# Kernel optimization log

Measured on AMD Instinct MI355X. Metric: run time of the kernel, lower is better.

The kernel has to match this reference:

```python
import jax, jax.numpy as jnp
import numpy as np

NE, NR = 100000, 50
E, H, M = 512, 8, 8
HD = E // H
B = 65536


def setup_inputs() -> dict:
    key = jax.random.key(0)
    ks = jax.random.split(key, 24)
    xav = lambda k, shp: jax.random.normal(k, shp, jnp.float32) * (2.0 / (shp[0] + shp[-1])) ** 0.5
    return {
        'entity_emb': xav(ks[0], (NE, E)),
        'relation_emb': xav(ks[1], (NR, E)),
        'dens_ent_emb': jax.random.normal(ks[2], (NE, E), jnp.float32) * 0.02,
        'dens_ent_w': xav(ks[3], (E, 1)), 'dens_ent_b': jnp.zeros((1,), jnp.float32),
        'dens_rel_emb': jax.random.normal(ks[4], (NR, E), jnp.float32) * 0.02,
        'dens_rel_w': xav(ks[5], (E, 1)), 'dens_rel_b': jnp.zeros((1,), jnp.float32),
        'local_motifs': xav(ks[6], (M, HD)),
        'global_motifs': xav(ks[7], (M, HD)),
        'Wq': xav(ks[8], (E, E)), 'bq': jnp.zeros((E,), jnp.float32),
        'Wkl': xav(ks[9], (HD, HD)), 'bkl': jnp.zeros((HD,), jnp.float32),
        'Wkg': xav(ks[10], (HD, HD)), 'bkg': jnp.zeros((HD,), jnp.float32),
        'Wout': xav(ks[11], (2 * E, E)), 'bout': jnp.zeros((E,), jnp.float32),
        'adv_w': jnp.float32(1.0), 'adv_b': jnp.float32(0.0),
        'h_idx': jax.random.randint(ks[12], (B,), 0, NE),
        'r_idx': jax.random.randint(ks[13], (B,), 0, NR),
        't_idx': jax.random.randint(ks[14], (B,), 0, NE),
    }


def reference(entity_emb, relation_emb, dens_ent_emb, dens_ent_w, dens_ent_b,
              dens_rel_emb, dens_rel_w, dens_rel_b, local_motifs, global_motifs,
              Wq, bq, Wkl, bkl, Wkg, bkg, Wout, bout, adv_w, adv_b,
              h_idx, r_idx, t_idx):
    h = entity_emb[h_idx]           # [B, E]
    r = relation_emb[r_idx]
    t = entity_emb[t_idx]
    # density gating: sigmoid(Linear(Embedding(idx))) per head/tail/relation, averaged
    h_d = jax.nn.sigmoid(dens_ent_emb[h_idx] @ dens_ent_w + dens_ent_b)   # [B,1]
    t_d = jax.nn.sigmoid(dens_ent_emb[t_idx] @ dens_ent_w + dens_ent_b)
    r_d = jax.nn.sigmoid(dens_rel_emb[r_idx] @ dens_rel_w + dens_rel_b)
    density = (h_d + t_d + r_d) / 3.0                                     # [B,1]
    diff = h + r - t
    # hierarchical soft attention over local/global motif codebooks
    ctx = h + r + t
    q = (ctx @ Wq + bq).reshape(-1, H, HD)                                # [B,H,HD]
    lk = local_motifs @ Wkl + bkl                                         # [M,HD]
    gk = global_motifs @ Wkg + bkg
    scale = 1.0 / jnp.sqrt(jnp.asarray(HD, q.dtype))
    dens = density[:, :, None]                                            # [B,1,1]
    l_w = jax.nn.softmax(jnp.einsum('bhd,md->bhm', q, lk) * scale + dens, axis=-1)
    g_w = jax.nn.softmax(jnp.einsum('bhd,md->bhm', q, gk) * scale + dens, axis=-1)
    attn = (l_w + g_w) / 2.0                                              # [B,H,M]
    motifs = local_motifs + global_motifs                                 # [M,HD]
    motif_repr = jnp.einsum('bhm,md->bhd', attn, motifs).reshape(-1, E)   # [B,E]
    motif_loss = jnp.sum((diff - motif_repr) ** 2, axis=-1)               # ||.||^2
    combined = jnp.concatenate([diff, motif_repr], axis=-1)               # [B,2E]
    transformed = jnp.tanh(combined @ Wout + bout)
    score = adv_w * jnp.linalg.norm(transformed, axis=-1) + adv_b
    return score, motif_loss
```

## Files before the change

kernel.cpp:

```cpp
#include <hip/hip_runtime.h>
#include <math.h>

#define B_TOT 65536

typedef __attribute__((ext_vector_type(4))) float f32x4;
typedef __attribute__((ext_vector_type(4))) unsigned int u32x4;
typedef __attribute__((ext_vector_type(8))) __bf16 bf16x8;

#define OFF_WLOGT 0u
#define OFF_CBIAS 131072u
#define OFF_BCAT  131584u
#define OFF_MOTIF 721408u
#define OFF_LK    723456u
#define OFF_GK    725504u
#define OFF_DIFF  1048576u
#define OFF_ATTN  68157440u
#define OFF_SSQ   76546048u

__device__ __forceinline__ unsigned short f2bf(float x) {
  union { float f; unsigned int u; } v; v.f = x;
  return (unsigned short)((v.u + 0x7FFFu + ((v.u >> 16) & 1u)) >> 16);
}

__device__ __forceinline__ float bf2f(unsigned short u) {
  union { unsigned int i; float f; } v; v.i = ((unsigned int)u) << 16; return v.f;
}

__device__ __forceinline__ float fast_tanh(float x) {
  float cx = fminf(fmaxf(x, -15.f), 15.f);
  float e = __expf(2.f * cx);
  return 1.f - 2.f * __builtin_amdgcn_rcpf(e + 1.f);
}

__global__ __launch_bounds__(256) void k0a(
    const float* __restrict__ lm, const float* __restrict__ gm,
    const float* __restrict__ Wkl, const float* __restrict__ bkl,
    const float* __restrict__ Wkg, const float* __restrict__ bkg,
    const float* __restrict__ bq,
    float* __restrict__ lk, float* __restrict__ gk,
    float* __restrict__ motifs, float* __restrict__ cb) {
  int tid = threadIdx.x;
  for (int o = tid; o < 512; o += 256) {
    int m = o >> 6, d = o & 63;
    float s1 = bkl[d], s2 = bkg[d];
    for (int k = 0; k < 64; ++k) {
      s1 += lm[m*64+k] * Wkl[k*64+d];
      s2 += gm[m*64+k] * Wkg[k*64+d];
    }
    lk[o] = s1; gk[o] = s2;
    motifs[o] = lm[o] + gm[o];
  }
  __syncthreads();
  if (tid < 128) {
    int s_ = tid >> 6, h = (tid >> 3) & 7, m = tid & 7;
    const float* K = s_ ? gk : lk;
    float s = 0.f;
    for (int d = 0; d < 64; ++d) s += bq[h*64+d] * K[m*64+d];
    cb[tid] = 0.125f * s;
  }
}

__global__ __launch_bounds__(256) void k0b(
    const float* __restrict__ Wq, const float* __restrict__ Wout,
    const float* __restrict__ lk, const float* __restrict__ gk,
    const float* __restrict__ motifs,
    unsigned short* __restrict__ wlogT, unsigned short* __restrict__ bcatT) {
  int idx = blockIdx.x * 256 + threadIdx.x;
  if (idx >= 65536 + 512*576) return;
  if (idx < 65536) {
    int c = idx >> 9, k = idx & 511;
    int s_ = c >> 6, h = (c >> 3) & 7, m = c & 7;
    const float* K = (s_ ? gk : lk) + m*64;
    const float* wq = Wq + (size_t)k*512 + h*64;
    float s = 0.f;
    for (int d = 0; d < 64; ++d) s += wq[d] * K[d];
    wlogT[(size_t)c*512 + k] = f2bf(0.125f * s);
  } else {
    int i2 = idx - 65536;
    int n = i2 / 576, k = i2 - n*576;
    float v;
    if (k < 512) {
      v = Wout[(size_t)k*512 + n];
    } else {
      int hm = k - 512, h = hm >> 3, m = hm & 7;
      const float* mo = motifs + m*64;
      const float* wo = Wout + (size_t)(512 + h*64)*512 + n;
      v = 0.f;
      for (int d = 0; d < 64; ++d) v += mo[d] * wo[(size_t)d*512];
    }
    bcatT[(size_t)n*576 + k] = f2bf(v);
  }
}

__global__ __launch_bounds__(256, 4) void kA(
    const float* __restrict__ ent, const float* __restrict__ rel,
    const int* __restrict__ hI, const int* __restrict__ rI, const int* __restrict__ tI,
    const unsigned short* __restrict__ wlogT, const float* __restrict__ cb,
    unsigned short* __restrict__ diffB, unsigned short* __restrict__ attnB) {
  __shared__ __align__(16) unsigned char smem[32768];
  unsigned short* As = (unsigned short*)smem;
  unsigned short* Bs = (unsigned short*)(smem + 9216);
  float* lg  = (float*)smem;

  int tid = threadIdx.x;
  int l = tid & 63, wid = tid >> 6;
  int wr = wid >> 1, wc = wid & 1;
  int rowBase = blockIdx.x * 64;
  int r_loc = tid >> 2, p = tid & 3;
  int b = rowBase + r_loc;

  int hi = hI[b], ri = rI[b], ti = tI[b];
  const float* hp = ent + (size_t)hi * 512;
  const float* tp = ent + (size_t)ti * 512;
  const float* rp = rel + (size_t)ri * 512;
  int bn = tid >> 1, half = tid & 1;
  const unsigned short* wsrc = wlogT + (size_t)bn * 512 + half * 32;

  f32x4 acc[2][4] = {};

  float4 gh[4], gt[4], gr[4];
  u32x4 wb[4];

  {
    int q0 = p*8, q1 = 32 + p*8;
    gh[0] = *(const float4*)(hp + q0); gh[1] = *(const float4*)(hp + q0 + 4);
    gh[2] = *(const float4*)(hp + q1); gh[3] = *(const float4*)(hp + q1 + 4);
    gt[0] = *(const float4*)(tp + q0); gt[1] = *(const float4*)(tp + q0 + 4);
    gt[2] = *(const float4*)(tp + q1); gt[3] = *(const float4*)(tp + q1 + 4);
    gr[0] = *(const float4*)(rp + q0); gr[1] = *(const float4*)(rp + q0 + 4);
    gr[2] = *(const float4*)(rp + q1); gr[3] = *(const float4*)(rp + q1 + 4);
    #pragma unroll
    for (int o = 0; o < 4; ++o) wb[o] = *(const u32x4*)(wsrc + o*8);
  }

  #pragma unroll
  for (int c = 0; c < 8; ++c) {
    int k0 = c * 64;
    union { u32x4 v[2]; unsigned short s[16]; } pd, pc;
    #pragma unroll
    for (int g = 0; g < 4; ++g) {
      #pragma unroll
      for (int j = 0; j < 4; ++j) {
        float hv = ((const float*)&gh[g])[j];
        float tv = ((const float*)&gt[g])[j];
        float rv = ((const float*)&gr[g])[j];
        pd.s[g*4+j] = f2bf(hv + rv - tv);
        pc.s[g*4+j] = f2bf(hv + rv + tv);
      }
    }

    __syncthreads();
    *(u32x4*)(As + r_loc*72 + p*8)      = pc.v[0];
    *(u32x4*)(As + r_loc*72 + 32 + p*8) = pc.v[1];
    {
      unsigned short* bp = Bs + bn*72 + half*32;
      *(u32x4*)(bp)      = wb[0];
      *(u32x4*)(bp + 8)  = wb[1];
      *(u32x4*)(bp + 16) = wb[2];
      *(u32x4*)(bp + 24) = wb[3];
    }
    *(u32x4*)(diffB + (size_t)b*512 + k0 + p*8)      = pd.v[0];
    *(u32x4*)(diffB + (size_t)b*512 + k0 + 32 + p*8) = pd.v[1];
    __syncthreads();
    if (c < 7) {
      int q0 = k0 + 64 + p*8, q1 = k0 + 96 + p*8;
      gh[0] = *(const float4*)(hp + q0); gh[1] = *(const float4*)(hp + q0 + 4);
      gh[2] = *(const float4*)(hp + q1); gh[3] = *(const float4*)(hp + q1 + 4);
      gt[0] = *(const float4*)(tp + q0); gt[1] = *(const float4*)(tp + q0 + 4);
      gt[2] = *(const float4*)(tp + q1); gt[3] = *(const float4*)(tp + q1 + 4);
      gr[0] = *(const float4*)(rp + q0); gr[1] = *(const float4*)(rp + q0 + 4);
      gr[2] = *(const float4*)(rp + q1); gr[3] = *(const float4*)(rp + q1 + 4);
      #pragma unroll
      for (int o = 0; o < 4; ++o) wb[o] = *(const u32x4*)(wsrc + (c+1)*64 + o*8);
    }
    #pragma unroll
    for (int kf = 0; kf < 2; ++kf) {
      bf16x8 af0 = *(const bf16x8*)(As + (wr*32 +      (l & 15))*72 + kf*32 + 8*(l >> 4));
      bf16x8 af1 = *(const bf16x8*)(As + (wr*32 + 16 + (l & 15))*72 + kf*32 + 8*(l >> 4));
      #pragma unroll
      for (int n = 0; n < 4; ++n) {
        bf16x8 bfr = *(const bf16x8*)(Bs + (wc*64 + n*16 + (l & 15))*72 + kf*32 + 8*(l >> 4));
        acc[0][n] = __builtin_amdgcn_mfma_f32_16x16x32_bf16(af0, bfr, acc[0][n], 0, 0, 0);
        acc[1][n] = __builtin_amdgcn_mfma_f32_16x16x32_bf16(af1, bfr, acc[1][n], 0, 0, 0);
      }
    }
  }

  __syncthreads();
  #pragma unroll
  for (int m = 0; m < 2; ++m)
    #pragma unroll
    for (int n = 0; n < 4; ++n)
      #pragma unroll
      for (int j = 0; j < 4; ++j) {
        int rr = wr*32 + m*16 + 4*(l >> 4) + j;
        int cc = wc*64 + n*16 + (l & 15);
        lg[rr*128 + ((cc + rr) & 127)] = acc[m][n][j];
      }
  __syncthreads();

  #pragma unroll
  for (int e = 0; e < 2; ++e) {
    int h = 2*p + e;
    float a8[8];
    #pragma unroll
    for (int m = 0; m < 8; ++m) a8[m] = 0.f;
    #pragma unroll
    for (int s = 0; s < 2; ++s) {
      float v[8], mx = -1e30f;
      #pragma unroll
      for (int m = 0; m < 8; ++m) {
        int cc = s*64 + h*8 + m;
        v[m] = lg[r_loc*128 + ((cc + r_loc) & 127)] + cb[cc];
        mx = fmaxf(mx, v[m]);
      }
      float sum = 0.f;
      #pragma unroll
      for (int m = 0; m < 8; ++m) { v[m] = __expf(v[m] - mx); sum += v[m]; }
      float inv = 0.5f / sum;
      #pragma unroll
      for (int m = 0; m < 8; ++m) a8[m] += v[m] * inv;
    }
    union { u32x4 v; unsigned short s[8]; } pk;
    #pragma unroll
    for (int m = 0; m < 8; ++m) pk.s[m] = f2bf(a8[m]);
    *(u32x4*)(attnB + (size_t)b*64 + h*8) = pk.v;
  }
}

__global__ __launch_bounds__(512, 4) void kB(
    const unsigned short* __restrict__ diffB, const unsigned short* __restrict__ attnB,
    const unsigned short* __restrict__ bcatT, const float* __restrict__ bout,
    float* __restrict__ ssqPart) {
  __shared__ __align__(16) unsigned short As[128*72];
  __shared__ __align__(16) unsigned short Bs[256*72];
  __shared__ float part[128*4];
  int tid = threadIdx.x;
  int l = tid & 63, wid = tid >> 6;
  int wr = wid >> 2, wc = wid & 3;
  int mblk = blockIdx.x >> 1, nblk = blockIdx.x & 1;
  int rowBase = mblk * 128;
  int colBase = nblk * 256;
  f32x4 acc[4][4] = {};
  int ar = tid >> 2, aq = tid & 3;
  int bn2 = tid >> 1, half = tid & 1;

  u32x4 na0, na1, nb0, nb1, nb2, nb3;
  {
    const unsigned short* ap = diffB + (size_t)(rowBase + ar)*512 + aq*16;
    na0 = *(const u32x4*)ap; na1 = *(const u32x4*)(ap + 8);
    const u32x4* src = (const u32x4*)(bcatT + (size_t)(colBase + bn2)*576 + half*32);
    nb0 = src[0]; nb1 = src[1]; nb2 = src[2]; nb3 = src[3];
  }
  for (int ks = 0; ks < 9; ++ks) {
    __syncthreads();
    *(u32x4*)(&As[ar*72 + aq*16])     = na0;
    *(u32x4*)(&As[ar*72 + aq*16 + 8]) = na1;
    {
      unsigned short* bp = &Bs[bn2*72 + half*32];
      *(u32x4*)(bp)      = nb0;
      *(u32x4*)(bp + 8)  = nb1;
      *(u32x4*)(bp + 16) = nb2;
      *(u32x4*)(bp + 24) = nb3;
    }
    __syncthreads();
    if (ks < 8) {
      int k0 = (ks + 1) * 64;
      const unsigned short* ap = (k0 < 512)
        ? diffB + (size_t)(rowBase + ar)*512 + k0 + aq*16
        : attnB + (size_t)(rowBase + ar)*64 + aq*16;
      na0 = *(const u32x4*)ap; na1 = *(const u32x4*)(ap + 8);
      const u32x4* src = (const u32x4*)(bcatT + (size_t)(colBase + bn2)*576 + k0 + half*32);
      nb0 = src[0]; nb1 = src[1]; nb2 = src[2]; nb3 = src[3];
    }
    #pragma unroll
    for (int kf = 0; kf < 2; ++kf) {
      bf16x8 af[4];
      #pragma unroll
      for (int m = 0; m < 4; ++m)
        af[m] = *(const bf16x8*)(&As[(wr*64 + m*16 + (l & 15))*72 + kf*32 + 8*(l >> 4)]);
      #pragma unroll
      for (int n = 0; n < 4; ++n) {
        bf16x8 bfr = *(const bf16x8*)(&Bs[(wc*64 + n*16 + (l & 15))*72 + kf*32 + 8*(l >> 4)]);
        #pragma unroll
        for (int m = 0; m < 4; ++m)
          acc[m][n] = __builtin_amdgcn_mfma_f32_16x16x32_bf16(af[m], bfr, acc[m][n], 0, 0, 0);
      }
    }
  }
  __syncthreads();
  float bo[4];
  #pragma unroll
  for (int n = 0; n < 4; ++n) bo[n] = bout[colBase + wc*64 + n*16 + (l & 15)];
  #pragma unroll
  for (int m = 0; m < 4; ++m) {
    float ss0 = 0.f, ss1 = 0.f, ss2 = 0.f, ss3 = 0.f;
    #pragma unroll
    for (int n = 0; n < 4; ++n) {
      float t0 = fast_tanh(acc[m][n][0] + bo[n]); ss0 += t0*t0;
      float t1 = fast_tanh(acc[m][n][1] + bo[n]); ss1 += t1*t1;
      float t2 = fast_tanh(acc[m][n][2] + bo[n]); ss2 += t2*t2;
      float t3 = fast_tanh(acc[m][n][3] + bo[n]); ss3 += t3*t3;
    }
    #pragma unroll
    for (int mask = 1; mask < 16; mask <<= 1) {
      ss0 += __shfl_xor(ss0, mask, 64);
      ss1 += __shfl_xor(ss1, mask, 64);
      ss2 += __shfl_xor(ss2, mask, 64);
      ss3 += __shfl_xor(ss3, mask, 64);
    }
    if ((l & 15) == 0) {
      int rbase = wr*64 + m*16 + (l >> 4)*4;
      part[(rbase+0)*4 + wc] = ss0;
      part[(rbase+1)*4 + wc] = ss1;
      part[(rbase+2)*4 + wc] = ss2;
      part[(rbase+3)*4 + wc] = ss3;
    }
  }
  __syncthreads();
  if (tid < 128) {
    float s = part[tid*4] + part[tid*4+1] + part[tid*4+2] + part[tid*4+3];
    ssqPart[(size_t)nblk*B_TOT + rowBase + tid] = s;
  }
}

__global__ __launch_bounds__(256) void kCD(
    const unsigned short* __restrict__ diffB, const unsigned short* __restrict__ attnB,
    const float* __restrict__ motifs, const float* __restrict__ ssqPart,
    const float* __restrict__ advw, const float* __restrict__ advb,
    float* __restrict__ lossOut, float* __restrict__ scoreOut) {
  __shared__ float mo[512];
  int tid = threadIdx.x;
  mo[tid] = motifs[tid];
  mo[tid + 256] = motifs[tid + 256];
  __syncthreads();
  int l = tid & 63;
  int b = blockIdx.x * 4 + (tid >> 6);
  union { u32x4 v; unsigned short s[8]; } dv, av;
  dv.v = *(const u32x4*)(diffB + (size_t)b*512 + l*8);
  int h = l >> 3;
  av.v = *(const u32x4*)(attnB + (size_t)b*64 + h*8);
  float at[8], df[8];
  #pragma unroll
  for (int j = 0; j < 8; ++j) { df[j] = bf2f(dv.s[j]); at[j] = bf2f(av.s[j]); }
  int dbase = (l & 7) * 8;
  float part = 0.f;
  #pragma unroll
  for (int j = 0; j < 8; ++j) {
    float repr = 0.f;
    #pragma unroll
    for (int m = 0; m < 8; ++m) repr += at[m] * mo[m*64 + dbase + j];
    float e = df[j] - repr;
    part += e * e;
  }
  #pragma unroll
  for (int off = 1; off < 64; off <<= 1) part += __shfl_xor(part, off, 64);
  if (l == 0) lossOut[b] = part;
  if (tid < 4) {
    int rb = blockIdx.x * 4 + tid;
    float s = ssqPart[rb] + ssqPart[B_TOT + rb];
    scoreOut[rb] = advw[0] * sqrtf(s) + advb[0];
  }
}

extern "C" void kernel_launch(void* const* d_in, const int* in_sizes, int n_in,
                              void* d_out, int out_size, void* d_ws, size_t ws_size,
                              hipStream_t stream) {
  const float* ent  = (const float*)d_in[0];
  const float* rel  = (const float*)d_in[1];
  const float* lm   = (const float*)d_in[8];
  const float* gm   = (const float*)d_in[9];
  const float* Wq   = (const float*)d_in[10];
  const float* bq   = (const float*)d_in[11];
  const float* Wkl  = (const float*)d_in[12];
  const float* bkl  = (const float*)d_in[13];
  const float* Wkg  = (const float*)d_in[14];
  const float* bkg  = (const float*)d_in[15];
  const float* Wout = (const float*)d_in[16];
  const float* bout = (const float*)d_in[17];
  const float* advw = (const float*)d_in[18];
  const float* advb = (const float*)d_in[19];
  const int* hI = (const int*)d_in[20];
  const int* rI = (const int*)d_in[21];
  const int* tI = (const int*)d_in[22];
  char* ws = (char*)d_ws;
  unsigned short* wlogT = (unsigned short*)(ws + OFF_WLOGT);
  float* cb     = (float*)(ws + OFF_CBIAS);
  unsigned short* bcatT = (unsigned short*)(ws + OFF_BCAT);
  float* motifs = (float*)(ws + OFF_MOTIF);
  float* lk     = (float*)(ws + OFF_LK);
  float* gk     = (float*)(ws + OFF_GK);
  unsigned short* diffB = (unsigned short*)(ws + OFF_DIFF);
  unsigned short* attnB = (unsigned short*)(ws + OFF_ATTN);
  float* ssqPart = (float*)(ws + OFF_SSQ);
  float* scoreOut = (float*)d_out;
  float* lossOut  = (float*)d_out + B_TOT;

  hipLaunchKernelGGL(k0a, dim3(1), dim3(256), 0, stream,
                     lm, gm, Wkl, bkl, Wkg, bkg, bq, lk, gk, motifs, cb);
  hipLaunchKernelGGL(k0b, dim3(1408), dim3(256), 0, stream,
                     Wq, Wout, lk, gk, motifs, wlogT, bcatT);
  hipLaunchKernelGGL(kA, dim3(B_TOT/64), dim3(256), 0, stream,
                     ent, rel, hI, rI, tI, wlogT, cb, diffB, attnB);
  hipLaunchKernelGGL(kB, dim3(B_TOT/128 * 2), dim3(512), 0, stream,
                     diffB, attnB, bcatT, bout, ssqPart);
  hipLaunchKernelGGL(kCD, dim3(B_TOT/4), dim3(256), 0, stream,
                     diffB, attnB, motifs, ssqPart, advw, advb, lossOut, scoreOut);
}
```

Measured before the change: 149.3 us.

## Shrink kA row tile to 32 rows for higher occupancy and more blocks

Kernel kA now processes 32 batch rows per block instead of 64, with eight threads per row each gathering 8 floats per chunk, and all four waves splitting the 128 logit columns. Shared memory drops to about 23 KB, register arrays shrink, and launch bounds rise to 6 blocks per CU, so more waves are resident to hide the random-gather latency. The cost is that the Wq-derived weight tile is loaded into LDS twice as often across the grid, and each block has less MFMA work per barrier.

```diff
diff --git a/kernel.cpp b/kernel.cpp
--- a/kernel.cpp
+++ b/kernel.cpp
@@ -92,21 +92,20 @@
   }
 }
 
-__global__ __launch_bounds__(256, 4) void kA(
+__global__ __launch_bounds__(256, 6) void kA(
     const float* __restrict__ ent, const float* __restrict__ rel,
     const int* __restrict__ hI, const int* __restrict__ rI, const int* __restrict__ tI,
     const unsigned short* __restrict__ wlogT, const float* __restrict__ cb,
     unsigned short* __restrict__ diffB, unsigned short* __restrict__ attnB) {
-  __shared__ __align__(16) unsigned char smem[32768];
+  __shared__ __align__(16) unsigned char smem[23040];
   unsigned short* As = (unsigned short*)smem;
-  unsigned short* Bs = (unsigned short*)(smem + 9216);
+  unsigned short* Bs = (unsigned short*)(smem + 4608);
   float* lg  = (float*)smem;
 
   int tid = threadIdx.x;
-  int l = tid & 63, wid = tid >> 6;
-  int wr = wid >> 1, wc = wid & 1;
-  int rowBase = blockIdx.x * 64;
-  int r_loc = tid >> 2, p = tid & 3;
+  int l = tid & 63, wc = tid >> 6;
+  int rowBase = blockIdx.x * 32;
+  int r_loc = tid >> 3, p = tid & 7;
   int b = rowBase + r_loc;
 
   int hi = hI[b], ri = rI[b], ti = tI[b];
@@ -116,19 +115,16 @@
   int bn = tid >> 1, half = tid & 1;
   const unsigned short* wsrc = wlogT + (size_t)bn * 512 + half * 32;
 
-  f32x4 acc[2][4] = {};
-
-  float4 gh[4], gt[4], gr[4];
+  f32x4 acc[2][2] = {};
+
+  float4 gh[2], gt[2], gr[2];
   u32x4 wb[4];
 
   {
-    int q0 = p*8, q1 = 32 + p*8;
+    int q0 = p*8;
     gh[0] = *(const float4*)(hp + q0); gh[1] = *(const float4*)(hp + q0 + 4);
-    gh[2] = *(const float4*)(hp + q1); gh[3] = *(const float4*)(hp + q1 + 4);
     gt[0] = *(const float4*)(tp + q0); gt[1] = *(const float4*)(tp + q0 + 4);
-    gt[2] = *(const float4*)(tp + q1); gt[3] = *(const float4*)(tp + q1 + 4);
     gr[0] = *(const float4*)(rp + q0); gr[1] = *(const float4*)(rp + q0 + 4);
-    gr[2] = *(const float4*)(rp + q1); gr[3] = *(const float4*)(rp + q1 + 4);
     #pragma unroll
     for (int o = 0; o < 4; ++o) wb[o] = *(const u32x4*)(wsrc + o*8);
   }
@@ -136,9 +132,9 @@
   #pragma unroll
   for (int c = 0; c < 8; ++c) {
     int k0 = c * 64;
-    union { u32x4 v[2]; unsigned short s[16]; } pd, pc;
-    #pragma unroll
-    for (int g = 0; g < 4; ++g) {
+    union { u32x4 v; unsigned short s[8]; } pd, pc;
+    #pragma unroll
+    for (int g = 0; g < 2; ++g) {
       #pragma unroll
       for (int j = 0; j < 4; ++j) {
         float hv = ((const float*)&gh[g])[j];
@@ -150,8 +146,7 @@
     }
 
     __syncthreads();
-    *(u32x4*)(As + r_loc*72 + p*8)      = pc.v[0];
-    *(u32x4*)(As + r_loc*72 + 32 + p*8) = pc.v[1];
+    *(u32x4*)(As + r_loc*72 + p*8) = pc.v;
     {
       unsigned short* bp = Bs + bn*72 + half*32;
       *(u32x4*)(bp)      = wb[0];
@@ -159,27 +154,24 @@
       *(u32x4*)(bp + 16) = wb[2];
       *(u32x4*)(bp + 24) = wb[3];
     }
-    *(u32x4*)(diffB + (size_t)b*512 + k0 + p*8)      = pd.v[0];
-    *(u32x4*)(diffB + (size_t)b*512 + k0 + 32 + p*8) = pd.v[1];
+    *(u32x4*)(diffB + (size_t)b*512 + k0 + p*8) = pd.v;
     __syncthreads();
     if (c < 7) {
-      int q0 = k0 + 64 + p*8, q1 = k0 + 96 + p*8;
+      int q0 = k0 + 64 + p*8;
       gh[0] = *(const float4*)(hp + q0); gh[1] = *(const float4*)(hp + q0 + 4);
-      gh[2] = *(const float4*)(hp + q1); gh[3] = *(const float4*)(hp + q1 + 4);
       gt[0] = *(const float4*)(tp + q0); gt[1] = *(const float4*)(tp + q0 + 4);
-      gt[2] = *(const float4*)(tp + q1); gt[3] = *(const float4*)(tp + q1 + 4);
       gr[0] = *(const float4*)(rp + q0); gr[1] = *(const float4*)(rp + q0 + 4);
-      gr[2] = *(const float4*)(rp + q1); gr[3] = *(const float4*)(rp + q1 + 4);
       #pragma unroll
       for (int o = 0; o < 4; ++o) wb[o] = *(const u32x4*)(wsrc + (c+1)*64 + o*8);
     }
     #pragma unroll
     for (int kf = 0; kf < 2; ++kf) {
-      bf16x8 af0 = *(const bf16x8*)(As + (wr*32 +      (l & 15))*72 + kf*32 + 8*(l >> 4));
-      bf16x8 af1 = *(const bf16x8*)(As + (wr*32 + 16 + (l & 15))*72 + kf*32 + 8*(l >> 4));
-      #pragma unroll
-      for (int n = 0; n < 4; ++n) {
-        bf16x8 bfr = *(const bf16x8*)(Bs + (wc*64 + n*16 + (l & 15))*72 + kf*32 + 8*(l >> 4));
+      bf16x8 af0 = *(const bf16x8*)(As + (     (l & 15))*72 + kf*32 + 8*(l >> 4));
+      bf16x8 af1 = *(const bf16x8*)(As + (16 + (l & 15))*72 + kf*32 + 8*(l >> 4));
+      #pragma unroll
+      for (int n = 0; n < 2; ++n) {
+        int col = wc*32 + n*16 + (l & 15);
+        bf16x8 bfr = *(const bf16x8*)(Bs + col*72 + kf*32 + 8*(l >> 4));
         acc[0][n] = __builtin_amdgcn_mfma_f32_16x16x32_bf16(af0, bfr, acc[0][n], 0, 0, 0);
         acc[1][n] = __builtin_amdgcn_mfma_f32_16x16x32_bf16(af1, bfr, acc[1][n], 0, 0, 0);
       }
@@ -190,18 +182,16 @@
   #pragma unroll
   for (int m = 0; m < 2; ++m)
     #pragma unroll
-    for (int n = 0; n < 4; ++n)
+    for (int n = 0; n < 2; ++n)
       #pragma unroll
       for (int j = 0; j < 4; ++j) {
-        int rr = wr*32 + m*16 + 4*(l >> 4) + j;
-        int cc = wc*64 + n*16 + (l & 15);
+        int rr = m*16 + 4*(l >> 4) + j;
+        int cc = wc*32 + n*16 + (l & 15);
         lg[rr*128 + ((cc + rr) & 127)] = acc[m][n][j];
       }
   __syncthreads();
 
-  #pragma unroll
-  for (int e = 0; e < 2; ++e) {
-    int h = 2*p + e;
+  {
     float a8[8];
     #pragma unroll
     for (int m = 0; m < 8; ++m) a8[m] = 0.f;
@@ -210,7 +200,7 @@
       float v[8], mx = -1e30f;
       #pragma unroll
       for (int m = 0; m < 8; ++m) {
-        int cc = s*64 + h*8 + m;
+        int cc = s*64 + p*8 + m;
         v[m] = lg[r_loc*128 + ((cc + r_loc) & 127)] + cb[cc];
         mx = fmaxf(mx, v[m]);
       }
@@ -224,7 +214,7 @@
     union { u32x4 v; unsigned short s[8]; } pk;
     #pragma unroll
     for (int m = 0; m < 8; ++m) pk.s[m] = f2bf(a8[m]);
-    *(u32x4*)(attnB + (size_t)b*64 + h*8) = pk.v;
+    *(u32x4*)(attnB + (size_t)b*64 + p*8) = pk.v;
   }
 }
 
@@ -400,7 +390,7 @@
                      lm, gm, Wkl, bkl, Wkg, bkg, bq, lk, gk, motifs, cb);
   hipLaunchKernelGGL(k0b, dim3(1408), dim3(256), 0, stream,
                      Wq, Wout, lk, gk, motifs, wlogT, bcatT);
-  hipLaunchKernelGGL(kA, dim3(B_TOT/64), dim3(256), 0, stream,
+  hipLaunchKernelGGL(kA, dim3(B_TOT/32), dim3(256), 0, stream,
                      ent, rel, hI, rI, tI, wlogT, cb, diffB, attnB);
   hipLaunchKernelGGL(kB, dim3(B_TOT/128 * 2), dim3(512), 0, stream,
                      diffB, attnB, bcatT, bout, ssqPart);
```

Measured after the change: 151.1 us. Within noise of the previous version (+1.1%).
